# Optimization experiments

Measured on AMD Instinct MI355X. Metric: run time of the kernel, lower is better.

Reference implementation:

```python
import jax, jax.numpy as jnp
import numpy as np

B, C, H, W = 16, 256, 128, 128
C4, COUT = C // 4, 256


def setup_inputs() -> dict:
    key = jax.random.key(0)
    ks = jax.random.split(key, 8)
    s = 0.05
    flow = jax.random.normal(ks[0], (B, C, H, W), jnp.float32)
    de_out = jax.random.normal(ks[1], (B, C, H, W), jnp.float32)
    Wq = jax.random.normal(ks[2], (C4, C), jnp.float32) * s
    bq = jax.random.normal(ks[3], (C4,), jnp.float32) * s
    Wk = jax.random.normal(ks[4], (C4, C), jnp.float32) * s
    bk = jax.random.normal(ks[5], (C4,), jnp.float32) * s
    Wv = jax.random.normal(ks[6], (COUT, C), jnp.float32) * s
    bv = jax.random.normal(ks[7], (COUT,), jnp.float32) * s
    return {"flow": flow, "de_out": de_out, "Wq": Wq, "bq": bq,
            "Wk": Wk, "bk": bk, "Wv": Wv, "bv": bv}


def reference(flow, de_out, Wq, bq, Wk, bk, Wv, bv):
    # 1x1 convs == per-pixel channel matmuls
    q = jnp.einsum('bchw,dc->bdhw', de_out, Wq) + bq[None, :, None, None]  # [B,C4,H,W]
    k = jnp.einsum('bchw,dc->bdhw', flow, Wk) + bk[None, :, None, None]    # [B,C4,H,W]
    v = jnp.einsum('bchw,dc->bdhw', flow, Wv) + bv[None, :, None, None]    # [B,COUT,H,W]
    # height-axis attention per (batch, width) column
    energy = jnp.einsum('bdhw,bdgw->bwhg', q, k)          # [B,W,H,H], g = key height
    att = jax.nn.softmax(energy, axis=-1)                  # softmax over key height
    out = jnp.einsum('bcgw,bwhg->bchw', v, att)            # [B,COUT,H,W]
    return out
```

## Files before the change

kernel.cpp:

```cpp
#include <hip/hip_runtime.h>
#include <cstdint>
#include <cstddef>

typedef unsigned short u16;
using half4 = __attribute__((ext_vector_type(4))) _Float16;
using half8 = __attribute__((ext_vector_type(8))) _Float16;
using f32x4 = __attribute__((ext_vector_type(4))) float;
using f4    = __attribute__((ext_vector_type(4))) float;

#define B_    16
#define C_    256
#define H_    128
#define W_    128
#define C4_   64
#define COUT_ 256
#define HW_   (H_ * W_)

#define LDS_S1    264
#define QK_S      72
#define P_S       136
#define XP_S      140

#define Q_ELEMS   ((size_t)B_ * W_ * H_ * C4_)
#define V_ELEMS   ((size_t)B_ * W_ * H_ * COUT_)
#define W16_ELEMS ((size_t)(C4_ * C_ + C4_ * C_ + COUT_ * C_))
#define WS_NEED   ((2 * Q_ELEMS + 2 * V_ELEMS + W16_ELEMS) * 2)

__device__ __forceinline__ u16 f16_rn(float f) {
  _Float16 h = (_Float16)f;
  return __builtin_bit_cast(u16, h);
}

__global__ void __launch_bounds__(256) wconv_kernel(
    const float* __restrict__ Wk, const float* __restrict__ Wq,
    const float* __restrict__ Wv, u16* __restrict__ W16) {
  const int bid = blockIdx.x;
  const int t   = threadIdx.x;
  const float* src;
  u16* dst;
  int idx;
  if (bid < 16)      { src = Wk; dst = W16;                 idx = bid * 1024 + t * 4; }
  else if (bid < 32) { src = Wq; dst = W16 + C4_ * C_;      idx = (bid - 16) * 1024 + t * 4; }
  else               { src = Wv; dst = W16 + 2 * C4_ * C_;  idx = (bid - 32) * 1024 + t * 4; }
  f4 v = *reinterpret_cast<const f4*>(src + idx);
  half4 h;
#pragma unroll
  for (int i = 0; i < 4; ++i) h[i] = (_Float16)v[i];
  *reinterpret_cast<half4*>(dst + idx) = h;
}

__device__ __forceinline__ const half8* afrag(const u16* __restrict__ ldsT,
                                              int w16, int ks, int lg) {
  int oct = (ks * 4 + lg) ^ ((w16 >> 2) & 7);
  return reinterpret_cast<const half8*>(&ldsT[w16 * LDS_S1 + oct * 8]);
}

__device__ __forceinline__ const half8* whfrag(const u16* __restrict__ Wm16,
                                               int row, int ks, int lg) {
  return reinterpret_cast<const half8*>(Wm16 + (size_t)row * C_ + ks * 32 + lg * 8);
}

__device__ __forceinline__ void proj4(const u16* __restrict__ ldsT,
                                      const u16* __restrict__ Wm16,
                                      const float* __restrict__ bm,
                                      u16* __restrict__ dst,
                                      int b, int h, int w0, int wv, int col, int lg) {
  f32x4 zero = {0.f, 0.f, 0.f, 0.f};
  f32x4 acc[4];
#pragma unroll
  for (int i = 0; i < 4; ++i) acc[i] = zero;
#pragma unroll
  for (int ks = 0; ks < 8; ++ks) {
    const half8 bfr = *whfrag(Wm16, wv * 16 + col, ks, lg);
#pragma unroll
    for (int wt = 0; wt < 4; ++wt) {
      const half8 afr = *afrag(ldsT, wt * 16 + col, ks, lg);
      acc[wt] = __builtin_amdgcn_mfma_f32_16x16x32_f16(afr, bfr, acc[wt], 0, 0, 0);
    }
  }
  const float bias = bm[wv * 16 + col];
#pragma unroll
  for (int wt = 0; wt < 4; ++wt)
#pragma unroll
    for (int r = 0; r < 4; ++r) {
      int w = w0 + wt * 16 + lg * 4 + r;
      dst[(((size_t)b * W_ + w) * H_ + h) * C4_ + wv * 16 + col] =
          f16_rn(acc[wt][r] + bias);
    }
}

__global__ void __launch_bounds__(256, 3) qkv_kernel(
    const float* __restrict__ flow, const float* __restrict__ de_out,
    const u16* __restrict__ W16,
    const float* __restrict__ bq, const float* __restrict__ bk,
    const float* __restrict__ bv,
    u16* __restrict__ Qws, u16* __restrict__ Kws, u16* __restrict__ Vws) {
  __shared__ __align__(16) u16 ldsT[64 * LDS_S1];
  const int t    = threadIdx.x;
  const int bid  = blockIdx.x;
  const int g      = (bid & 7) | ((bid >> 6) << 3);
  const int hlow   = (bid >> 3) & 7;
  const int w0     = (g & 1) * 64;
  const int hgrp   = (g >> 1) & 15;
  const int b      = (g >> 5) & 15;
  const int srcsel = g >> 9;
  const int h      = hgrp * 8 + hlow;
  const int lane = t & 63;
  const int wv   = t >> 6;
  const int col  = lane & 15;
  const int lg   = lane >> 4;

  const u16* Wk16 = W16;
  const u16* Wq16 = W16 + C4_ * C_;
  const u16* Wv16 = W16 + 2 * C4_ * C_;

  const float* src =
      (srcsel ? de_out : flow) + (size_t)b * C_ * HW_ + (size_t)h * W_ + w0;

  f4 va[8], vb[8];
#pragma unroll
  for (int i = 0; i < 8; ++i) {
    const int u = i * 256 + t;
    const float* s0 = src + (size_t)(2 * (u >> 4)) * HW_ + (u & 15) * 4;
    va[i] = *reinterpret_cast<const f4*>(s0);
    vb[i] = *reinterpret_cast<const f4*>(s0 + HW_);
  }
#pragma unroll
  for (int i = 0; i < 8; ++i) {
    const int u = i * 256 + t;
    const int c = 2 * (u >> 4);
    const int q = u & 15;
#pragma unroll
    for (int j = 0; j < 4; ++j) {
      const int w   = q * 4 + j;
      const int oct = (c >> 3) ^ (q & 7);
      uint32_t pk = (uint32_t)f16_rn(va[i][j]) | ((uint32_t)f16_rn(vb[i][j]) << 16);
      *reinterpret_cast<uint32_t*>(&ldsT[w * LDS_S1 + oct * 8 + (c & 7)]) = pk;
    }
  }
  __syncthreads();

  if (srcsel == 0) {
    proj4(ldsT, Wk16, bk, Kws, b, h, w0, wv, col, lg);
    f32x4 zero = {0.f, 0.f, 0.f, 0.f};
    f32x4 acc[4][4];
#pragma unroll
    for (int j = 0; j < 4; ++j)
#pragma unroll
      for (int i = 0; i < 4; ++i) acc[j][i] = zero;
#pragma unroll
    for (int ks = 0; ks < 8; ++ks) {
      half8 bfr[4];
#pragma unroll
      for (int j = 0; j < 4; ++j)
        bfr[j] = *whfrag(Wv16, (wv * 4 + j) * 16 + col, ks, lg);
#pragma unroll
      for (int wt = 0; wt < 4; ++wt) {
        const half8 afr = *afrag(ldsT, wt * 16 + col, ks, lg);
#pragma unroll
        for (int j = 0; j < 4; ++j)
          acc[j][wt] =
              __builtin_amdgcn_mfma_f32_16x16x32_f16(afr, bfr[j], acc[j][wt], 0, 0, 0);
      }
    }
#pragma unroll
    for (int j = 0; j < 4; ++j) {
      const int co = (wv * 4 + j) * 16 + col;
      const float bias = bv[co];
#pragma unroll
      for (int wt = 0; wt < 4; ++wt)
#pragma unroll
        for (int r = 0; r < 4; ++r) {
          int w = w0 + wt * 16 + lg * 4 + r;
          Vws[(size_t)(b * W_ + w) * 32768 + ((h >> 3) * COUT_ + co) * 8 + (h & 7)] =
              f16_rn(acc[j][wt][r] + bias);
        }
    }
  } else {
    proj4(ldsT, Wq16, bq, Qws, b, h, w0, wv, col, lg);
  }
}

template <int EPI>
__global__ void __launch_bounds__(256) attn_kernel(
    const u16* __restrict__ Qws, const u16* __restrict__ Kws,
    const u16* __restrict__ Vws, u16* __restrict__ out_tmp,
    float* __restrict__ out) {
  __shared__ __align__(16) u16 ldsQK[2 * 128 * QK_S];

  const int t   = threadIdx.x;
  const int bid = blockIdx.x;
  const int sw  = (bid & 7) * 256 + (bid >> 3);
  const int b   = sw >> 7;
  const int w   = sw & 127;
  const int lane = t & 63;
  const int wv   = t >> 6;
  const int col  = lane & 15;
  const int lg   = lane >> 4;

  const u16* qc    = Qws + ((size_t)b * W_ + w) * H_ * C4_;
  const u16* kc    = Kws + ((size_t)b * W_ + w) * H_ * C4_;
  const u16* vbase = Vws + (size_t)(b * W_ + w) * 32768;

  u16* ldsQ = ldsQK;
  u16* ldsK = ldsQK + 128 * QK_S;

#pragma unroll
  for (int i = 0; i < 4; ++i) {
    int item = i * 256 + t;
    int hh   = item >> 3;
    int d0   = (item & 7) * 8;
    *reinterpret_cast<half8*>(&ldsQ[hh * QK_S + d0]) =
        *reinterpret_cast<const half8*>(qc + item * 8);
    *reinterpret_cast<half8*>(&ldsK[hh * QK_S + d0]) =
        *reinterpret_cast<const half8*>(kc + item * 8);
  }
  __syncthreads();

  f32x4 zero = {0.f, 0.f, 0.f, 0.f};
  f32x4 e[2][8];
#pragma unroll
  for (int ht = 0; ht < 2; ++ht)
#pragma unroll
    for (int gt = 0; gt < 8; ++gt) e[ht][gt] = zero;

#pragma unroll
  for (int ks = 0; ks < 2; ++ks) {
    half8 aq[2];
#pragma unroll
    for (int ht = 0; ht < 2; ++ht)
      aq[ht] = *reinterpret_cast<const half8*>(
          &ldsQ[(wv * 32 + ht * 16 + col) * QK_S + ks * 32 + lg * 8]);
#pragma unroll
    for (int gt = 0; gt < 8; ++gt) {
      const half8 bk_ = *reinterpret_cast<const half8*>(
          &ldsK[(gt * 16 + col) * QK_S + ks * 32 + lg * 8]);
#pragma unroll
      for (int ht = 0; ht < 2; ++ht)
        e[ht][gt] = __builtin_amdgcn_mfma_f32_16x16x32_f16(aq[ht], bk_, e[ht][gt], 0, 0, 0);
    }
  }
  __syncthreads();

  u16* ldsP = ldsQK + wv * 32 * P_S;

#pragma unroll
  for (int ht = 0; ht < 2; ++ht)
#pragma unroll
    for (int r = 0; r < 4; ++r) {
      float m = -1e30f;
#pragma unroll
      for (int gt = 0; gt < 8; ++gt) m = fmaxf(m, e[ht][gt][r]);
#pragma unroll
      for (int off = 1; off < 16; off <<= 1) m = fmaxf(m, __shfl_xor(m, off));
      float s = 0.f;
#pragma unroll
      for (int gt = 0; gt < 8; ++gt) {
        float p = __expf(e[ht][gt][r] - m);
        e[ht][gt][r] = p;
        s += p;
      }
#pragma unroll
      for (int off = 1; off < 16; off <<= 1) s += __shfl_xor(s, off);
      const float inv = 1.f / s;
      const int hh = ht * 16 + lg * 4 + r;
#pragma unroll
      for (int gt = 0; gt < 8; ++gt)
        ldsP[hh * P_S + gt * 16 + col] = f16_rn(e[ht][gt][r] * inv);
    }

  f32x4 o[2][16];
#pragma unroll
  for (int ht = 0; ht < 2; ++ht)
#pragma unroll
    for (int ct = 0; ct < 16; ++ct) o[ht][ct] = zero;

#pragma unroll
  for (int ks = 0; ks < 4; ++ks) {
    half8 ap[2];
#pragma unroll
    for (int ht = 0; ht < 2; ++ht)
      ap[ht] = *reinterpret_cast<const half8*>(
          &ldsP[(ht * 16 + col) * P_S + ks * 32 + lg * 8]);
#pragma unroll
    for (int ct = 0; ct < 16; ++ct) {
      const half8 bv_ = *reinterpret_cast<const half8*>(
          vbase + ((ks * 4 + lg) * COUT_ + ct * 16 + col) * 8);
#pragma unroll
      for (int ht = 0; ht < 2; ++ht)
        o[ht][ct] = __builtin_amdgcn_mfma_f32_16x16x32_f16(ap[ht], bv_, o[ht][ct], 0, 0, 0);
    }
  }

  if (EPI == 1) {
    u16* ldsX = ldsQK;
    u16* dst_col = out_tmp + ((size_t)(b * W_ + w) << 15);
#pragma unroll
    for (int ctg = 0; ctg < 4; ++ctg) {
      __syncthreads();
#pragma unroll
      for (int j = 0; j < 4; ++j) {
        const int ct    = ctg * 4 + j;
        const int c_loc = j * 16 + col;
#pragma unroll
        for (int ht = 0; ht < 2; ++ht) {
          const int hbase = wv * 32 + ht * 16 + lg * 4;
          half4 pk;
#pragma unroll
          for (int r = 0; r < 4; ++r) pk[r] = (_Float16)o[ht][ct][r];
          *reinterpret_cast<half4*>(&ldsX[c_loc * XP_S + hbase]) = pk;
        }
      }
      __syncthreads();
      const int c_loc = t >> 2;
      const int h0    = (t & 3) * 32;
      u16* dp = dst_col + (ctg * 64 + c_loc) * 128 + h0;
#pragma unroll
      for (int k = 0; k < 4; ++k)
        *reinterpret_cast<half8*>(dp + k * 8) =
            *reinterpret_cast<const half8*>(&ldsX[c_loc * XP_S + h0 + k * 8]);
    }
  } else {
    float* outp = out + (size_t)b * COUT_ * HW_ + w;
#pragma unroll
    for (int ht = 0; ht < 2; ++ht)
#pragma unroll
      for (int ct = 0; ct < 16; ++ct)
#pragma unroll
        for (int r = 0; r < 4; ++r) {
          int hrow = wv * 32 + ht * 16 + lg * 4 + r;
          int c = ct * 16 + col;
          outp[((size_t)c * H_ + hrow) * W_] = o[ht][ct][r];
        }
  }
}

__global__ void __launch_bounds__(256) transpose_kernel(
    const u16* __restrict__ T, float* __restrict__ out) {
  __shared__ float lds[64 * 132];
  const int t   = threadIdx.x;
  const int bid = blockIdx.x;
  const int b   = bid >> 9;
  const int ft  = bid & 511;

  {
    const int w  = t >> 1;
    const int fo = (t & 1) * 32;
    const u16* src = T + ((size_t)(b * W_ + w) << 15) + ft * 64 + fo;
#pragma unroll
    for (int k = 0; k < 4; ++k) {
      half8 v = *reinterpret_cast<const half8*>(src + k * 8);
#pragma unroll
      for (int e = 0; e < 8; ++e)
        lds[(fo + k * 8 + e) * 132 + w] = (float)v[e];
    }
  }
  __syncthreads();
  {
    const int f_loc = t >> 2;
    const int w0    = (t & 3) * 32;
    float* dst = out + (size_t)b * (COUT_ * HW_) + (size_t)(ft * 64 + f_loc) * 128 + w0;
#pragma unroll
    for (int k = 0; k < 8; ++k) {
      f4 v4;
#pragma unroll
      for (int e = 0; e < 4; ++e) v4[e] = lds[f_loc * 132 + w0 + k * 4 + e];
      *reinterpret_cast<f4*>(dst + k * 4) = v4;
    }
  }
}

extern "C" void kernel_launch(void* const* d_in, const int* in_sizes, int n_in,
                              void* d_out, int out_size, void* d_ws, size_t ws_size,
                              hipStream_t stream) {
  const float* flow   = (const float*)d_in[0];
  const float* de_out = (const float*)d_in[1];
  const float* Wq = (const float*)d_in[2];
  const float* bq = (const float*)d_in[3];
  const float* Wk = (const float*)d_in[4];
  const float* bk = (const float*)d_in[5];
  const float* Wv = (const float*)d_in[6];
  const float* bv = (const float*)d_in[7];
  float* out = (float*)d_out;

  u16* Qws = (u16*)d_ws;
  u16* Kws = Qws + Q_ELEMS;
  u16* Vws = Kws + Q_ELEMS;
  u16* W16 = Vws + V_ELEMS;
  u16* Tws = W16 + W16_ELEMS;

  wconv_kernel<<<96, 256, 0, stream>>>(Wk, Wq, Wv, W16);
  qkv_kernel<<<2 * B_ * H_ * 2, 256, 0, stream>>>(flow, de_out, W16, bq, bk, bv,
                                                  Qws, Kws, Vws);
  if (ws_size >= (size_t)WS_NEED) {
    attn_kernel<1><<<B_ * W_, 256, 0, stream>>>(Qws, Kws, Vws, Tws, out);
    transpose_kernel<<<B_ * 512, 256, 0, stream>>>(Tws, out);
  } else {
    attn_kernel<0><<<B_ * W_, 256, 0, stream>>>(Qws, Kws, Vws, Tws, out);
  }
}
```

Measured before the change: 552.3 us.

## Stage QKV input via global_load_lds in quarters and coalesce Q/K stores through LDS

```diff
diff --git a/kernel.cpp b/kernel.cpp
--- a/kernel.cpp
+++ b/kernel.cpp
@@ -20,6 +20,7 @@
 #define QK_S      72
 #define P_S       136
 #define XP_S      140
+#define O_S       72
 
 #define Q_ELEMS   ((size_t)B_ * W_ * H_ * C4_)
 #define V_ELEMS   ((size_t)B_ * W_ * H_ * COUT_)
@@ -29,6 +30,12 @@
 __device__ __forceinline__ u16 f16_rn(float f) {
   _Float16 h = (_Float16)f;
   return __builtin_bit_cast(u16, h);
+}
+
+__device__ __forceinline__ void gload16(const void* g, void* l) {
+  __builtin_amdgcn_global_load_lds(
+      (const __attribute__((address_space(1))) void*)g,
+      (__attribute__((address_space(3))) void*)l, 16, 0, 0);
 }
 
 __global__ void __launch_bounds__(256) wconv_kernel(
@@ -49,44 +56,15 @@
   *reinterpret_cast<half4*>(dst + idx) = h;
 }
 
-__device__ __forceinline__ const half8* afrag(const u16* __restrict__ ldsT,
+__device__ __forceinline__ const half8* afrag(const u16* __restrict__ T,
                                               int w16, int ks, int lg) {
   int oct = (ks * 4 + lg) ^ ((w16 >> 2) & 7);
-  return reinterpret_cast<const half8*>(&ldsT[w16 * LDS_S1 + oct * 8]);
+  return reinterpret_cast<const half8*>(&T[w16 * LDS_S1 + oct * 8]);
 }
 
 __device__ __forceinline__ const half8* whfrag(const u16* __restrict__ Wm16,
                                                int row, int ks, int lg) {
   return reinterpret_cast<const half8*>(Wm16 + (size_t)row * C_ + ks * 32 + lg * 8);
-}
-
-__device__ __forceinline__ void proj4(const u16* __restrict__ ldsT,
-                                      const u16* __restrict__ Wm16,
-                                      const float* __restrict__ bm,
-                                      u16* __restrict__ dst,
-                                      int b, int h, int w0, int wv, int col, int lg) {
-  f32x4 zero = {0.f, 0.f, 0.f, 0.f};
-  f32x4 acc[4];
-#pragma unroll
-  for (int i = 0; i < 4; ++i) acc[i] = zero;
-#pragma unroll
-  for (int ks = 0; ks < 8; ++ks) {
-    const half8 bfr = *whfrag(Wm16, wv * 16 + col, ks, lg);
-#pragma unroll
-    for (int wt = 0; wt < 4; ++wt) {
-      const half8 afr = *afrag(ldsT, wt * 16 + col, ks, lg);
-      acc[wt] = __builtin_amdgcn_mfma_f32_16x16x32_f16(afr, bfr, acc[wt], 0, 0, 0);
-    }
-  }
-  const float bias = bm[wv * 16 + col];
-#pragma unroll
-  for (int wt = 0; wt < 4; ++wt)
-#pragma unroll
-    for (int r = 0; r < 4; ++r) {
-      int w = w0 + wt * 16 + lg * 4 + r;
-      dst[(((size_t)b * W_ + w) * H_ + h) * C4_ + wv * 16 + col] =
-          f16_rn(acc[wt][r] + bias);
-    }
 }
 
 __global__ void __launch_bounds__(256, 3) qkv_kernel(
@@ -95,7 +73,11 @@
     const float* __restrict__ bq, const float* __restrict__ bk,
     const float* __restrict__ bv,
     u16* __restrict__ Qws, u16* __restrict__ Kws, u16* __restrict__ Vws) {
-  __shared__ __align__(16) u16 ldsT[64 * LDS_S1];
+  __shared__ __align__(16) unsigned char ldsraw[16384 + 64 * LDS_S1 * 2];
+  float* F = reinterpret_cast<float*>(ldsraw);
+  u16*   T = reinterpret_cast<u16*>(ldsraw + 16384);
+  u16*   O = reinterpret_cast<u16*>(ldsraw);
+
   const int t    = threadIdx.x;
   const int bid  = blockIdx.x;
   const int g      = (bid & 7) | ((bid >> 6) << 3);
@@ -117,32 +99,68 @@
   const float* src =
       (srcsel ? de_out : flow) + (size_t)b * C_ * HW_ + (size_t)h * W_ + w0;
 
-  f4 va[8], vb[8];
-#pragma unroll
-  for (int i = 0; i < 8; ++i) {
-    const int u = i * 256 + t;
-    const float* s0 = src + (size_t)(2 * (u >> 4)) * HW_ + (u & 15) * 4;
-    va[i] = *reinterpret_cast<const f4*>(s0);
-    vb[i] = *reinterpret_cast<const f4*>(s0 + HW_);
-  }
-#pragma unroll
-  for (int i = 0; i < 8; ++i) {
-    const int u = i * 256 + t;
-    const int c = 2 * (u >> 4);
-    const int q = u & 15;
-#pragma unroll
-    for (int j = 0; j < 4; ++j) {
-      const int w   = q * 4 + j;
-      const int oct = (c >> 3) ^ (q & 7);
-      uint32_t pk = (uint32_t)f16_rn(va[i][j]) | ((uint32_t)f16_rn(vb[i][j]) << 16);
-      *reinterpret_cast<uint32_t*>(&ldsT[w * LDS_S1 + oct * 8 + (c & 7)]) = pk;
-    }
-  }
-  __syncthreads();
+  for (int qtr = 0; qtr < 4; ++qtr) {
+    const float* s = src + (size_t)(qtr * 64) * HW_;
+#pragma unroll
+    for (int i = 0; i < 4; ++i) {
+      const int rr0 = wv * 16 + i * 4;
+      gload16(s + (size_t)(rr0 + (lane >> 4)) * HW_ + (lane & 15) * 4,
+              F + rr0 * 64);
+    }
+    __syncthreads();
+#pragma unroll
+    for (int i = 0; i < 2; ++i) {
+      const int flat = i * 256 + t;
+      const int wq = flat & 15;
+      const int pp = flat >> 4;
+      const f4 fa = *reinterpret_cast<const f4*>(&F[(2 * pp) * 64 + wq * 4]);
+      const f4 fb = *reinterpret_cast<const f4*>(&F[(2 * pp + 1) * 64 + wq * 4]);
+      const int c   = qtr * 64 + 2 * pp;
+      const int oct = (c >> 3) ^ (wq & 7);
+#pragma unroll
+      for (int j = 0; j < 4; ++j) {
+        const int w = wq * 4 + j;
+        uint32_t pk = (uint32_t)f16_rn(fa[j]) | ((uint32_t)f16_rn(fb[j]) << 16);
+        *reinterpret_cast<uint32_t*>(&T[w * LDS_S1 + oct * 8 + (c & 7)]) = pk;
+      }
+    }
+    __syncthreads();
+  }
 
   if (srcsel == 0) {
-    proj4(ldsT, Wk16, bk, Kws, b, h, w0, wv, col, lg);
     f32x4 zero = {0.f, 0.f, 0.f, 0.f};
+    {
+      f32x4 acc[4];
+#pragma unroll
+      for (int i = 0; i < 4; ++i) acc[i] = zero;
+#pragma unroll
+      for (int ks = 0; ks < 8; ++ks) {
+        const half8 bfr = *whfrag(Wk16, wv * 16 + col, ks, lg);
+#pragma unroll
+        for (int wt = 0; wt < 4; ++wt) {
+          const half8 afr = *afrag(T, wt * 16 + col, ks, lg);
+          acc[wt] = __builtin_amdgcn_mfma_f32_16x16x32_f16(afr, bfr, acc[wt], 0, 0, 0);
+        }
+      }
+      const float bias = bk[wv * 16 + col];
+#pragma unroll
+      for (int wt = 0; wt < 4; ++wt)
+#pragma unroll
+        for (int r = 0; r < 4; ++r)
+          O[(wt * 16 + lg * 4 + r) * O_S + wv * 16 + col] = f16_rn(acc[wt][r] + bias);
+    }
+    __syncthreads();
+    {
+#pragma unroll
+      for (int i = 0; i < 2; ++i) {
+        const int item = i * 256 + t;
+        const int wl = item >> 3;
+        const int d0 = (item & 7) * 8;
+        *reinterpret_cast<half8*>(
+            &Kws[(((size_t)b * W_ + w0 + wl) * H_ + h) * C4_ + d0]) =
+            *reinterpret_cast<const half8*>(&O[wl * O_S + d0]);
+      }
+    }
     f32x4 acc[4][4];
 #pragma unroll
     for (int j = 0; j < 4; ++j)
@@ -156,7 +174,7 @@
         bfr[j] = *whfrag(Wv16, (wv * 4 + j) * 16 + col, ks, lg);
 #pragma unroll
       for (int wt = 0; wt < 4; ++wt) {
-        const half8 afr = *afrag(ldsT, wt * 16 + col, ks, lg);
+        const half8 afr = *afrag(T, wt * 16 + col, ks, lg);
 #pragma unroll
         for (int j = 0; j < 4; ++j)
           acc[j][wt] =
@@ -177,7 +195,37 @@
         }
     }
   } else {
-    proj4(ldsT, Wq16, bq, Qws, b, h, w0, wv, col, lg);
+    f32x4 zero = {0.f, 0.f, 0.f, 0.f};
+    f32x4 acc[4];
+#pragma unroll
+    for (int i = 0; i < 4; ++i) acc[i] = zero;
+#pragma unroll
+    for (int ks = 0; ks < 8; ++ks) {
+      const half8 bfr = *whfrag(Wq16, wv * 16 + col, ks, lg);
+#pragma unroll
+      for (int wt = 0; wt < 4; ++wt) {
+        const half8 afr = *afrag(T, wt * 16 + col, ks, lg);
+        acc[wt] = __builtin_amdgcn_mfma_f32_16x16x32_f16(afr, bfr, acc[wt], 0, 0, 0);
+      }
+    }
+    const float bias = bq[wv * 16 + col];
+#pragma unroll
+    for (int wt = 0; wt < 4; ++wt)
+#pragma unroll
+      for (int r = 0; r < 4; ++r)
+        O[(wt * 16 + lg * 4 + r) * O_S + wv * 16 + col] = f16_rn(acc[wt][r] + bias);
+    __syncthreads();
+    {
+#pragma unroll
+      for (int i = 0; i < 2; ++i) {
+        const int item = i * 256 + t;
+        const int wl = item >> 3;
+        const int d0 = (item & 7) * 8;
+        *reinterpret_cast<half8*>(
+            &Qws[(((size_t)b * W_ + w0 + wl) * H_ + h) * C4_ + d0]) =
+            *reinterpret_cast<const half8*>(&O[wl * O_S + d0]);
+      }
+    }
   }
 }
 
```

Result: no change. 547.6 us (-0.9%).

## Transpose inputs to fp16 column-major, then fuse QKV projection into attention kernel

Applied to the files above, without the earlier changes.

```diff
diff --git a/kernel.cpp b/kernel.cpp
--- a/kernel.cpp
+++ b/kernel.cpp
@@ -7,6 +7,7 @@
 using half8 = __attribute__((ext_vector_type(8))) _Float16;
 using f32x4 = __attribute__((ext_vector_type(4))) float;
 using f4    = __attribute__((ext_vector_type(4))) float;
+using u32x4 = __attribute__((ext_vector_type(4))) uint32_t;
 
 #define B_    16
 #define C_    256
@@ -16,15 +17,14 @@
 #define COUT_ 256
 #define HW_   (H_ * W_)
 
-#define LDS_S1    264
-#define QK_S      72
-#define P_S       136
-#define XP_S      140
-
-#define Q_ELEMS   ((size_t)B_ * W_ * H_ * C4_)
-#define V_ELEMS   ((size_t)B_ * W_ * H_ * COUT_)
+#define QK_S  72
+#define P_S   136
+#define XP_S  140
+#define VT_SO 2056
+
+#define XT_HALF   ((size_t)B_ * W_ * H_ * C_)
 #define W16_ELEMS ((size_t)(C4_ * C_ + C4_ * C_ + COUT_ * C_))
-#define WS_NEED   ((2 * Q_ELEMS + 2 * V_ELEMS + W16_ELEMS) * 2)
+#define WS_NEED   ((2 * XT_HALF + W16_ELEMS) * 2)
 
 __device__ __forceinline__ u16 f16_rn(float f) {
   _Float16 h = (_Float16)f;
@@ -49,10 +49,50 @@
   *reinterpret_cast<half4*>(dst + idx) = h;
 }
 
-__device__ __forceinline__ const half8* afrag(const u16* __restrict__ ldsT,
-                                              int w16, int ks, int lg) {
-  int oct = (ks * 4 + lg) ^ ((w16 >> 2) & 7);
-  return reinterpret_cast<const half8*>(&ldsT[w16 * LDS_S1 + oct * 8]);
+__global__ void __launch_bounds__(256) xt_kernel(
+    const float* __restrict__ flow, const float* __restrict__ de_out,
+    u16* __restrict__ XT) {
+  __shared__ uint32_t Lw[128 * 36];
+  const int t   = threadIdx.x;
+  const int bid = blockIdx.x;
+  const int cq  = bid & 3;
+  const int h   = (bid >> 2) & 127;
+  const int b   = (bid >> 9) & 15;
+  const int src = bid >> 13;
+
+  const float* in = (src ? de_out : flow) +
+                    (size_t)b * C_ * HW_ + (size_t)(cq * 64) * HW_ + (size_t)h * W_;
+
+#pragma unroll
+  for (int it = 0; it < 4; ++it) {
+    const int c2 = it * 8 + (t >> 5);
+    const int w4 = (t & 31) * 4;
+    const float* r0 = in + (size_t)(2 * c2) * HW_ + w4;
+    f4 va = *reinterpret_cast<const f4*>(r0);
+    f4 vb = *reinterpret_cast<const f4*>(r0 + HW_);
+#pragma unroll
+    for (int j = 0; j < 4; ++j) {
+      const int w  = w4 + j;
+      const int sw = ((w >> 2) & 7) * 4;
+      Lw[w * 36 + (c2 ^ sw)] =
+          (uint32_t)f16_rn(va[j]) | ((uint32_t)f16_rn(vb[j]) << 16);
+    }
+  }
+  __syncthreads();
+
+  {
+    const int w     = t >> 1;
+    const int chalf = t & 1;
+    const int sw    = ((w >> 2) & 7) * 4;
+    u16* dst = XT + (size_t)src * XT_HALF +
+               (((size_t)(b * W_ + w)) * H_ + h) * C_ + cq * 64 + chalf * 32;
+#pragma unroll
+    for (int k = 0; k < 4; ++k) {
+      const int c2b = (chalf * 16 + k * 4) ^ sw;
+      u32x4 v = *reinterpret_cast<const u32x4*>(&Lw[w * 36 + c2b]);
+      *reinterpret_cast<u32x4*>(dst + k * 8) = v;
+    }
+  }
 }
 
 __device__ __forceinline__ const half8* whfrag(const u16* __restrict__ Wm16,
@@ -60,133 +100,15 @@
   return reinterpret_cast<const half8*>(Wm16 + (size_t)row * C_ + ks * 32 + lg * 8);
 }
 
-__device__ __forceinline__ void proj4(const u16* __restrict__ ldsT,
-                                      const u16* __restrict__ Wm16,
-                                      const float* __restrict__ bm,
-                                      u16* __restrict__ dst,
-                                      int b, int h, int w0, int wv, int col, int lg) {
-  f32x4 zero = {0.f, 0.f, 0.f, 0.f};
-  f32x4 acc[4];
-#pragma unroll
-  for (int i = 0; i < 4; ++i) acc[i] = zero;
-#pragma unroll
-  for (int ks = 0; ks < 8; ++ks) {
-    const half8 bfr = *whfrag(Wm16, wv * 16 + col, ks, lg);
-#pragma unroll
-    for (int wt = 0; wt < 4; ++wt) {
-      const half8 afr = *afrag(ldsT, wt * 16 + col, ks, lg);
-      acc[wt] = __builtin_amdgcn_mfma_f32_16x16x32_f16(afr, bfr, acc[wt], 0, 0, 0);
-    }
-  }
-  const float bias = bm[wv * 16 + col];
-#pragma unroll
-  for (int wt = 0; wt < 4; ++wt)
-#pragma unroll
-    for (int r = 0; r < 4; ++r) {
-      int w = w0 + wt * 16 + lg * 4 + r;
-      dst[(((size_t)b * W_ + w) * H_ + h) * C4_ + wv * 16 + col] =
-          f16_rn(acc[wt][r] + bias);
-    }
-}
-
-__global__ void __launch_bounds__(256, 3) qkv_kernel(
-    const float* __restrict__ flow, const float* __restrict__ de_out,
+__global__ void __launch_bounds__(512) fused_kernel(
+    u16* XTbuf,
     const u16* __restrict__ W16,
     const float* __restrict__ bq, const float* __restrict__ bk,
-    const float* __restrict__ bv,
-    u16* __restrict__ Qws, u16* __restrict__ Kws, u16* __restrict__ Vws) {
-  __shared__ __align__(16) u16 ldsT[64 * LDS_S1];
-  const int t    = threadIdx.x;
-  const int bid  = blockIdx.x;
-  const int g      = (bid & 7) | ((bid >> 6) << 3);
-  const int hlow   = (bid >> 3) & 7;
-  const int w0     = (g & 1) * 64;
-  const int hgrp   = (g >> 1) & 15;
-  const int b      = (g >> 5) & 15;
-  const int srcsel = g >> 9;
-  const int h      = hgrp * 8 + hlow;
-  const int lane = t & 63;
-  const int wv   = t >> 6;
-  const int col  = lane & 15;
-  const int lg   = lane >> 4;
-
-  const u16* Wk16 = W16;
-  const u16* Wq16 = W16 + C4_ * C_;
-  const u16* Wv16 = W16 + 2 * C4_ * C_;
-
-  const float* src =
-      (srcsel ? de_out : flow) + (size_t)b * C_ * HW_ + (size_t)h * W_ + w0;
-
-  f4 va[8], vb[8];
-#pragma unroll
-  for (int i = 0; i < 8; ++i) {
-    const int u = i * 256 + t;
-    const float* s0 = src + (size_t)(2 * (u >> 4)) * HW_ + (u & 15) * 4;
-    va[i] = *reinterpret_cast<const f4*>(s0);
-    vb[i] = *reinterpret_cast<const f4*>(s0 + HW_);
-  }
-#pragma unroll
-  for (int i = 0; i < 8; ++i) {
-    const int u = i * 256 + t;
-    const int c = 2 * (u >> 4);
-    const int q = u & 15;
-#pragma unroll
-    for (int j = 0; j < 4; ++j) {
-      const int w   = q * 4 + j;
-      const int oct = (c >> 3) ^ (q & 7);
-      uint32_t pk = (uint32_t)f16_rn(va[i][j]) | ((uint32_t)f16_rn(vb[i][j]) << 16);
-      *reinterpret_cast<uint32_t*>(&ldsT[w * LDS_S1 + oct * 8 + (c & 7)]) = pk;
-    }
-  }
-  __syncthreads();
-
-  if (srcsel == 0) {
-    proj4(ldsT, Wk16, bk, Kws, b, h, w0, wv, col, lg);
-    f32x4 zero = {0.f, 0.f, 0.f, 0.f};
-    f32x4 acc[4][4];
-#pragma unroll
-    for (int j = 0; j < 4; ++j)
-#pragma unroll
-      for (int i = 0; i < 4; ++i) acc[j][i] = zero;
-#pragma unroll
-    for (int ks = 0; ks < 8; ++ks) {
-      half8 bfr[4];
-#pragma unroll
-      for (int j = 0; j < 4; ++j)
-        bfr[j] = *whfrag(Wv16, (wv * 4 + j) * 16 + col, ks, lg);
-#pragma unroll
-      for (int wt = 0; wt < 4; ++wt) {
-        const half8 afr = *afrag(ldsT, wt * 16 + col, ks, lg);
-#pragma unroll
-        for (int j = 0; j < 4; ++j)
-          acc[j][wt] =
-              __builtin_amdgcn_mfma_f32_16x16x32_f16(afr, bfr[j], acc[j][wt], 0, 0, 0);
-      }
-    }
-#pragma unroll
-    for (int j = 0; j < 4; ++j) {
-      const int co = (wv * 4 + j) * 16 + col;
-      const float bias = bv[co];
-#pragma unroll
-      for (int wt = 0; wt < 4; ++wt)
-#pragma unroll
-        for (int r = 0; r < 4; ++r) {
-          int w = w0 + wt * 16 + lg * 4 + r;
-          Vws[(size_t)(b * W_ + w) * 32768 + ((h >> 3) * COUT_ + co) * 8 + (h & 7)] =
-              f16_rn(acc[j][wt][r] + bias);
-        }
-    }
-  } else {
-    proj4(ldsT, Wq16, bq, Qws, b, h, w0, wv, col, lg);
-  }
-}
-
-template <int EPI>
-__global__ void __launch_bounds__(256) attn_kernel(
-    const u16* __restrict__ Qws, const u16* __restrict__ Kws,
-    const u16* __restrict__ Vws, u16* __restrict__ out_tmp,
-    float* __restrict__ out) {
-  __shared__ __align__(16) u16 ldsQK[2 * 128 * QK_S];
+    const float* __restrict__ bv) {
+  __shared__ __align__(16) u16 lds[2 * 128 * QK_S + 16 * VT_SO];
+  u16* ldsQ  = lds;
+  u16* ldsK  = lds + 128 * QK_S;
+  u16* ldsVT = lds + 2 * 128 * QK_S;
 
   const int t   = threadIdx.x;
   const int bid = blockIdx.x;
@@ -198,140 +120,163 @@
   const int col  = lane & 15;
   const int lg   = lane >> 4;
 
-  const u16* qc    = Qws + ((size_t)b * W_ + w) * H_ * C4_;
-  const u16* kc    = Kws + ((size_t)b * W_ + w) * H_ * C4_;
-  const u16* vbase = Vws + (size_t)(b * W_ + w) * 32768;
-
-  u16* ldsQ = ldsQK;
-  u16* ldsK = ldsQK + 128 * QK_S;
-
-#pragma unroll
-  for (int i = 0; i < 4; ++i) {
-    int item = i * 256 + t;
-    int hh   = item >> 3;
-    int d0   = (item & 7) * 8;
-    *reinterpret_cast<half8*>(&ldsQ[hh * QK_S + d0]) =
-        *reinterpret_cast<const half8*>(qc + item * 8);
-    *reinterpret_cast<half8*>(&ldsK[hh * QK_S + d0]) =
-        *reinterpret_cast<const half8*>(kc + item * 8);
+  const u16* xf = XTbuf + ((size_t)(b * W_) + w) * (H_ * C_);
+  u16*       xd = XTbuf + XT_HALF + ((size_t)(b * W_) + w) * (H_ * C_);
+
+  const u16* Wk16 = W16;
+  const u16* Wq16 = W16 + C4_ * C_;
+  const u16* Wv16 = W16 + 2 * C4_ * C_;
+
+  f32x4 zero = {0.f, 0.f, 0.f, 0.f};
+
+  half8 af[8];
+#pragma unroll
+  for (int ks = 0; ks < 8; ++ks)
+    af[ks] = *reinterpret_cast<const half8*>(
+        xf + (size_t)(wv * 16 + col) * C_ + ks * 32 + lg * 8);
+  {
+    f32x4 acck[4];
+#pragma unroll
+    for (int i = 0; i < 4; ++i) acck[i] = zero;
+#pragma unroll
+    for (int ks = 0; ks < 8; ++ks)
+#pragma unroll
+      for (int nt = 0; nt < 4; ++nt)
+        acck[nt] = __builtin_amdgcn_mfma_f32_16x16x32_f16(
+            af[ks], *whfrag(Wk16, nt * 16 + col, ks, lg), acck[nt], 0, 0, 0);
+#pragma unroll
+    for (int nt = 0; nt < 4; ++nt) {
+      const float bias = bk[nt * 16 + col];
+#pragma unroll
+      for (int r = 0; r < 4; ++r)
+        ldsK[(wv * 16 + lg * 4 + r) * QK_S + nt * 16 + col] =
+            f16_rn(acck[nt][r] + bias);
+    }
+  }
+  {
+    f32x4 accv[16];
+#pragma unroll
+    for (int i = 0; i < 16; ++i) accv[i] = zero;
+#pragma unroll
+    for (int ks = 0; ks < 8; ++ks)
+#pragma unroll
+      for (int nt = 0; nt < 16; ++nt)
+        accv[nt] = __builtin_amdgcn_mfma_f32_16x16x32_f16(
+            af[ks], *whfrag(Wv16, nt * 16 + col, ks, lg), accv[nt], 0, 0, 0);
+    const int goct = wv * 2 + (lg >> 1);
+    const int hl0  = (lg & 1) * 4;
+#pragma unroll
+    for (int nt = 0; nt < 16; ++nt) {
+      const int c = nt * 16 + col;
+      const float bias = bv[c];
+      half4 pk;
+#pragma unroll
+      for (int r = 0; r < 4; ++r) pk[r] = (_Float16)(accv[nt][r] + bias);
+      *reinterpret_cast<half4*>(&ldsVT[goct * VT_SO + c * 8 + hl0]) = pk;
+    }
+  }
+  {
+#pragma unroll
+    for (int ks = 0; ks < 8; ++ks)
+      af[ks] = *reinterpret_cast<const half8*>(
+          xd + (size_t)(wv * 16 + col) * C_ + ks * 32 + lg * 8);
+    f32x4 accq[4];
+#pragma unroll
+    for (int i = 0; i < 4; ++i) accq[i] = zero;
+#pragma unroll
+    for (int ks = 0; ks < 8; ++ks)
+#pragma unroll
+      for (int nt = 0; nt < 4; ++nt)
+        accq[nt] = __builtin_amdgcn_mfma_f32_16x16x32_f16(
+            af[ks], *whfrag(Wq16, nt * 16 + col, ks, lg), accq[nt], 0, 0, 0);
+#pragma unroll
+    for (int nt = 0; nt < 4; ++nt) {
+      const float bias = bq[nt * 16 + col];
+#pragma unroll
+      for (int r = 0; r < 4; ++r)
+        ldsQ[(wv * 16 + lg * 4 + r) * QK_S + nt * 16 + col] =
+            f16_rn(accq[nt][r] + bias);
+    }
   }
   __syncthreads();
 
-  f32x4 zero = {0.f, 0.f, 0.f, 0.f};
-  f32x4 e[2][8];
-#pragma unroll
-  for (int ht = 0; ht < 2; ++ht)
-#pragma unroll
-    for (int gt = 0; gt < 8; ++gt) e[ht][gt] = zero;
-
+  f32x4 e[8];
+#pragma unroll
+  for (int gt = 0; gt < 8; ++gt) e[gt] = zero;
 #pragma unroll
   for (int ks = 0; ks < 2; ++ks) {
-    half8 aq[2];
-#pragma unroll
-    for (int ht = 0; ht < 2; ++ht)
-      aq[ht] = *reinterpret_cast<const half8*>(
-          &ldsQ[(wv * 32 + ht * 16 + col) * QK_S + ks * 32 + lg * 8]);
+    const half8 aq = *reinterpret_cast<const half8*>(
+        &ldsQ[(wv * 16 + col) * QK_S + ks * 32 + lg * 8]);
 #pragma unroll
     for (int gt = 0; gt < 8; ++gt) {
-      const half8 bk_ = *reinterpret_cast<const half8*>(
+      const half8 bkf = *reinterpret_cast<const half8*>(
           &ldsK[(gt * 16 + col) * QK_S + ks * 32 + lg * 8]);
-#pragma unroll
-      for (int ht = 0; ht < 2; ++ht)
-        e[ht][gt] = __builtin_amdgcn_mfma_f32_16x16x32_f16(aq[ht], bk_, e[ht][gt], 0, 0, 0);
+      e[gt] = __builtin_amdgcn_mfma_f32_16x16x32_f16(aq, bkf, e[gt], 0, 0, 0);
     }
   }
   __syncthreads();
 
-  u16* ldsP = ldsQK + wv * 32 * P_S;
-
-#pragma unroll
-  for (int ht = 0; ht < 2; ++ht)
-#pragma unroll
-    for (int r = 0; r < 4; ++r) {
-      float m = -1e30f;
-#pragma unroll
-      for (int gt = 0; gt < 8; ++gt) m = fmaxf(m, e[ht][gt][r]);
-#pragma unroll
-      for (int off = 1; off < 16; off <<= 1) m = fmaxf(m, __shfl_xor(m, off));
-      float s = 0.f;
-#pragma unroll
-      for (int gt = 0; gt < 8; ++gt) {
-        float p = __expf(e[ht][gt][r] - m);
-        e[ht][gt][r] = p;
-        s += p;
-      }
-#pragma unroll
-      for (int off = 1; off < 16; off <<= 1) s += __shfl_xor(s, off);
-      const float inv = 1.f / s;
-      const int hh = ht * 16 + lg * 4 + r;
-#pragma unroll
-      for (int gt = 0; gt < 8; ++gt)
-        ldsP[hh * P_S + gt * 16 + col] = f16_rn(e[ht][gt][r] * inv);
-    }
-
-  f32x4 o[2][16];
-#pragma unroll
-  for (int ht = 0; ht < 2; ++ht)
-#pragma unroll
-    for (int ct = 0; ct < 16; ++ct) o[ht][ct] = zero;
-
+  u16* ldsP = lds;
+#pragma unroll
+  for (int r = 0; r < 4; ++r) {
+    float m = -1e30f;
+#pragma unroll
+    for (int gt = 0; gt < 8; ++gt) m = fmaxf(m, e[gt][r]);
+#pragma unroll
+    for (int off = 1; off < 16; off <<= 1) m = fmaxf(m, __shfl_xor(m, off));
+    float s = 0.f;
+#pragma unroll
+    for (int gt = 0; gt < 8; ++gt) {
+      float p = __expf(e[gt][r] - m);
+      e[gt][r] = p;
+      s += p;
+    }
+#pragma unroll
+    for (int off = 1; off < 16; off <<= 1) s += __shfl_xor(s, off);
+    const float inv = 1.f / s;
+    const int hh = wv * 16 + lg * 4 + r;
+#pragma unroll
+    for (int gt = 0; gt < 8; ++gt)
+      ldsP[hh * P_S + gt * 16 + col] = f16_rn(e[gt][r] * inv);
+  }
+
+  f32x4 o[16];
+#pragma unroll
+  for (int ct = 0; ct < 16; ++ct) o[ct] = zero;
 #pragma unroll
   for (int ks = 0; ks < 4; ++ks) {
-    half8 ap[2];
-#pragma unroll
-    for (int ht = 0; ht < 2; ++ht)
-      ap[ht] = *reinterpret_cast<const half8*>(
-          &ldsP[(ht * 16 + col) * P_S + ks * 32 + lg * 8]);
+    const half8 ap = *reinterpret_cast<const half8*>(
+        &ldsP[(wv * 16 + col) * P_S + ks * 32 + lg * 8]);
 #pragma unroll
     for (int ct = 0; ct < 16; ++ct) {
-      const half8 bv_ = *reinterpret_cast<const half8*>(
-          vbase + ((ks * 4 + lg) * COUT_ + ct * 16 + col) * 8);
-#pragma unroll
-      for (int ht = 0; ht < 2; ++ht)
-        o[ht][ct] = __builtin_amdgcn_mfma_f32_16x16x32_f16(ap[ht], bv_, o[ht][ct], 0, 0, 0);
-    }
-  }
-
-  if (EPI == 1) {
-    u16* ldsX = ldsQK;
-    u16* dst_col = out_tmp + ((size_t)(b * W_ + w) << 15);
-#pragma unroll
-    for (int ctg = 0; ctg < 4; ++ctg) {
-      __syncthreads();
-#pragma unroll
-      for (int j = 0; j < 4; ++j) {
-        const int ct    = ctg * 4 + j;
-        const int c_loc = j * 16 + col;
-#pragma unroll
-        for (int ht = 0; ht < 2; ++ht) {
-          const int hbase = wv * 32 + ht * 16 + lg * 4;
-          half4 pk;
-#pragma unroll
-          for (int r = 0; r < 4; ++r) pk[r] = (_Float16)o[ht][ct][r];
-          *reinterpret_cast<half4*>(&ldsX[c_loc * XP_S + hbase]) = pk;
-        }
-      }
-      __syncthreads();
-      const int c_loc = t >> 2;
-      const int h0    = (t & 3) * 32;
-      u16* dp = dst_col + (ctg * 64 + c_loc) * 128 + h0;
-#pragma unroll
-      for (int k = 0; k < 4; ++k)
-        *reinterpret_cast<half8*>(dp + k * 8) =
-            *reinterpret_cast<const half8*>(&ldsX[c_loc * XP_S + h0 + k * 8]);
-    }
-  } else {
-    float* outp = out + (size_t)b * COUT_ * HW_ + w;
-#pragma unroll
-    for (int ht = 0; ht < 2; ++ht)
-#pragma unroll
-      for (int ct = 0; ct < 16; ++ct)
-#pragma unroll
-        for (int r = 0; r < 4; ++r) {
-          int hrow = wv * 32 + ht * 16 + lg * 4 + r;
-          int c = ct * 16 + col;
-          outp[((size_t)c * H_ + hrow) * W_] = o[ht][ct][r];
-        }
+      const half8 bvf = *reinterpret_cast<const half8*>(
+          &ldsVT[(ks * 4 + lg) * VT_SO + (ct * 16 + col) * 8]);
+      o[ct] = __builtin_amdgcn_mfma_f32_16x16x32_f16(ap, bvf, o[ct], 0, 0, 0);
+    }
+  }
+
+  u16* ldsX = lds;
+  u16* dst_col = xd;
+#pragma unroll
+  for (int ctg = 0; ctg < 4; ++ctg) {
+    __syncthreads();
+#pragma unroll
+    for (int j = 0; j < 4; ++j) {
+      const int ct    = ctg * 4 + j;
+      const int c_loc = j * 16 + col;
+      half4 pk;
+#pragma unroll
+      for (int r = 0; r < 4; ++r) pk[r] = (_Float16)o[ct][r];
+      *reinterpret_cast<half4*>(&ldsX[c_loc * XP_S + wv * 16 + lg * 4]) = pk;
+    }
+    __syncthreads();
+    const int c_loc = t >> 3;
+    const int h0    = (t & 7) * 16;
+    u16* dp = dst_col + (ctg * 64 + c_loc) * 128 + h0;
+    *reinterpret_cast<half8*>(dp) =
+        *reinterpret_cast<const half8*>(&ldsX[c_loc * XP_S + h0]);
+    *reinterpret_cast<half8*>(dp + 8) =
+        *reinterpret_cast<const half8*>(&ldsX[c_loc * XP_S + h0 + 8]);
   }
 }
 
@@ -383,19 +328,11 @@
   const float* bv = (const float*)d_in[7];
   float* out = (float*)d_out;
 
-  u16* Qws = (u16*)d_ws;
-  u16* Kws = Qws + Q_ELEMS;
-  u16* Vws = Kws + Q_ELEMS;
-  u16* W16 = Vws + V_ELEMS;
-  u16* Tws = W16 + W16_ELEMS;
+  u16* XTws = (u16*)d_ws;
+  u16* W16  = XTws + 2 * XT_HALF;
 
   wconv_kernel<<<96, 256, 0, stream>>>(Wk, Wq, Wv, W16);
-  qkv_kernel<<<2 * B_ * H_ * 2, 256, 0, stream>>>(flow, de_out, W16, bq, bk, bv,
-                                                  Qws, Kws, Vws);
-  if (ws_size >= (size_t)WS_NEED) {
-    attn_kernel<1><<<B_ * W_, 256, 0, stream>>>(Qws, Kws, Vws, Tws, out);
-    transpose_kernel<<<B_ * 512, 256, 0, stream>>>(Tws, out);
-  } else {
-    attn_kernel<0><<<B_ * W_, 256, 0, stream>>>(Qws, Kws, Vws, Tws, out);
-  }
-}
+  xt_kernel<<<2 * B_ * H_ * 4, 256, 0, stream>>>(flow, de_out, XTws);
+  fused_kernel<<<B_ * W_, 512, 0, stream>>>(XTws, W16, bq, bk, bv);
+  transpose_kernel<<<B_ * 512, 256, 0, stream>>>(XTws + XT_HALF, out);
+}
```

Measured after the change: 694.8 us. +25.8%, slower.
